# Kernel optimization log

Measured on AMD Instinct MI355X. Metric: run time of the kernel, lower is better.

The kernel has to match this reference:

```python
import jax, jax.numpy as jnp
import numpy as np

V = 32000; EMB = 128; EH = 256; DH = 256; AD = 256; BN = 512
UNK, START, END, PAD = 0, 1, 2, 3
COV_FACTOR = 1.0
B, T_IN, T_TGT = 16, 400, 100


def _lstm_cell(x, h, c, Wih, Whh, b):
    # PyTorch gate order: i, f, g, o
    g = x @ Wih.T + h @ Whh.T + b
    i, f, gg, o = jnp.split(g, 4, axis=-1)
    c = jax.nn.sigmoid(f) * c + jax.nn.sigmoid(i) * jnp.tanh(gg)
    h = jax.nn.sigmoid(o) * jnp.tanh(c)
    return h, c


def _lstm_scan(xs, Wih, Whh, b):
    # xs: [T, B, Din]
    Bz, H = xs.shape[1], Whh.shape[-1]
    def step(carry, xt):
        h, c = _lstm_cell(xt, carry[0], carry[1], Wih, Whh, b)
        return (h, c), h
    init = (jnp.zeros((Bz, H), xs.dtype), jnp.zeros((Bz, H), xs.dtype))
    (hT, cT), hs = jax.lax.scan(step, init, xs)
    return hs, hT, cT


def _bilstm(x, Wih, Whh, b):
    # x: [B, T, Din]; Wih/Whh/b stacked over direction (fwd, bwd)
    xs = jnp.swapaxes(x, 0, 1)
    hf, hTf, cTf = _lstm_scan(xs, Wih[0], Whh[0], b[0])
    hb, hTb, cTb = _lstm_scan(xs[::-1], Wih[1], Whh[1], b[1])
    out = jnp.concatenate([hf, hb[::-1]], axis=-1)  # [T, B, 2H]
    return jnp.swapaxes(out, 0, 1), jnp.concatenate([hTf, hTb], -1), jnp.concatenate([cTf, cTb], -1)


def forward_loss(emb, enc_Wih0, enc_Whh0, enc_b0, enc_Wih1, enc_Whh1, enc_b1, W_e2dh, b_e2dh, W_e2dc, b_e2dc, dec_Wih0, dec_Whh0, dec_b0, dec_Wih1, dec_Whh1, dec_b1, W_enc_attn, b_enc_attn, W_dec_attn, w_cov, v_attn, W_v1, b_v1, W_v2, b_v2, w_ctx_sw, b_ctx_sw, w_dec_sw, w_emb_sw, input_ids, target_ids, target_lengths):
    Bz, Tt = target_ids.shape
    safe_in = jnp.where(input_ids >= V, UNK, input_ids)
    x0 = emb[safe_in]                                          # [B, T_in, EMB]
    h_seq, hT0, cT0 = _bilstm(x0, enc_Wih0, enc_Whh0, enc_b0)
    enc_states, hT1, cT1 = _bilstm(h_seq, enc_Wih1, enc_Whh1, enc_b1)  # [B, T_in, 2*EH]
    hT = jnp.stack([hT0, hT1])                                 # [2, B, 2*EH] (fwd||bwd per layer)
    cT = jnp.stack([cT0, cT1])
    dec_h = hT @ W_e2dh.T + b_e2dh                             # [2, B, DH]
    dec_c = cT @ W_e2dc.T + b_e2dc
    enc_attn = enc_states @ W_enc_attn.T + b_enc_attn          # precomputed, loop-invariant
    pad_mask = input_ids == PAD
    safe_tgt = jnp.where(target_ids >= V, UNK, target_ids)
    # teacher forcing: input at t=0 is <s>, then safe(target[t-1])
    tok_in = jnp.concatenate([jnp.full((Bz, 1), START, dtype=target_ids.dtype), safe_tgt[:, :-1]], axis=1)

    def step(carry, inp):
        dh, dc, coverage, nll, cov = carry
        tok_t, tgt_t, t = inp
        e = emb[tok_t]
        h0, c0 = _lstm_cell(e, dh[0], dc[0], dec_Wih0, dec_Whh0, dec_b0)
        h1, c1 = _lstm_cell(h0, dh[1], dc[1], dec_Wih1, dec_Whh1, dec_b1)
        feat = jnp.tanh(enc_attn + (h1 @ W_dec_attn.T)[:, None, :] + coverage[..., None] * w_cov)
        scores = jnp.where(pad_mask, -jnp.inf, feat @ v_attn)
        attn = jax.nn.softmax(scores, axis=1)                  # [B, T_in]
        ctx = jnp.einsum('bt,btd->bd', attn, enc_states)
        vd = jax.nn.softmax(jax.nn.relu(jnp.concatenate([h1, ctx], axis=1) @ W_v1.T + b_v1) @ W_v2.T + b_v2, axis=1)
        # extended vocab = END left-pad zeros + generation dist (max_num_oovs = 0)
        p_vocab = jnp.take_along_axis(jnp.pad(vd, ((0, 0), (END, 0))), tgt_t[:, None], axis=1)[:, 0]
        p_gen = jax.nn.sigmoid(ctx @ w_ctx_sw + b_ctx_sw[0] + h1 @ w_dec_sw + e @ w_emb_sw)
        p_copy = jnp.sum(attn * (input_ids == tgt_t[:, None]), axis=1)
        p = p_gen * p_vocab + (1.0 - p_gen) * p_copy
        active = t < target_lengths
        nll = nll - jnp.where(active, jnp.log(p + 1e-9), 0.0)
        cov = cov + jnp.where(active, jnp.sum(jnp.minimum(attn, coverage), axis=1), 0.0)
        return (jnp.stack([h0, h1]), jnp.stack([c0, c1]), coverage + attn, nll, cov), None

    init = (dec_h, dec_c, jnp.zeros(input_ids.shape, enc_states.dtype), jnp.zeros((Bz,), enc_states.dtype), jnp.zeros((Bz,), enc_states.dtype))
    (_, _, _, nll, cov), _ = jax.lax.scan(step, init, (tok_in.T, target_ids.T, jnp.arange(Tt)))
    nll_loss = nll.sum()
    cov_loss = cov.sum()
    return jnp.stack([nll_loss, cov_loss, nll_loss + COV_FACTOR * cov_loss])


def setup_inputs() -> dict:
    ks = iter(jax.random.split(jax.random.key(0), 48))
    def w(shape, scale=0.05):
        return (jax.random.normal(next(ks), shape) * scale).astype(jnp.float32)
    def lstm_b(*shape):
        b = np.zeros(shape, np.float32)
        n = shape[-1]
        b[..., n // 4: n // 2] = 1.0  # forget-gate bias = 1 as in init_weights
        return jnp.asarray(b)
    inp = {}
    inp['batch_input_ids'] = jax.random.randint(next(ks), (B, T_IN), 0, V)
    inp['batch_target_ids'] = jax.random.randint(next(ks), (B, T_TGT), 0, V)
    inp['input_lengths'] = jnp.full((B,), T_IN, dtype=jnp.int32)  # full-length batch
    inp['target_lengths'] = jax.random.randint(next(ks), (B,), 1, T_TGT + 1)
    inp['emb'] = w((V, EMB), 0.1)
    inp['enc_Wih0'] = w((2, 4 * EH, EMB)); inp['enc_Whh0'] = w((2, 4 * EH, EH)); inp['enc_b0'] = lstm_b(2, 4 * EH)
    inp['enc_Wih1'] = w((2, 4 * EH, 2 * EH)); inp['enc_Whh1'] = w((2, 4 * EH, EH)); inp['enc_b1'] = lstm_b(2, 4 * EH)
    inp['W_e2dh'] = w((DH, 2 * EH)); inp['b_e2dh'] = jnp.zeros((DH,), jnp.float32)
    inp['W_e2dc'] = w((DH, 2 * EH)); inp['b_e2dc'] = jnp.zeros((DH,), jnp.float32)
    inp['dec_Wih0'] = w((4 * DH, EMB)); inp['dec_Whh0'] = w((4 * DH, DH)); inp['dec_b0'] = lstm_b(4 * DH)
    inp['dec_Wih1'] = w((4 * DH, DH)); inp['dec_Whh1'] = w((4 * DH, DH)); inp['dec_b1'] = lstm_b(4 * DH)
    inp['W_enc_attn'] = w((AD, 2 * EH)); inp['b_enc_attn'] = jnp.zeros((AD,), jnp.float32)
    inp['W_dec_attn'] = w((AD, DH))
    inp['w_cov'] = w((AD,))
    inp['v_attn'] = w((AD,))
    inp['W_v1'] = w((BN, DH + 2 * EH)); inp['b_v1'] = jnp.zeros((BN,), jnp.float32)
    inp['W_v2'] = w((V - END, BN)); inp['b_v2'] = jnp.zeros((V - END,), jnp.float32)
    inp['w_ctx_sw'] = w((2 * EH,)); inp['b_ctx_sw'] = jnp.zeros((1,), jnp.float32)
    inp['w_dec_sw'] = w((DH,)); inp['w_emb_sw'] = w((EMB,))
    return inp


def reference(batch_input_ids, batch_target_ids, input_lengths, target_lengths, emb, enc_Wih0, enc_Whh0, enc_b0, enc_Wih1, enc_Whh1, enc_b1, W_e2dh, b_e2dh, W_e2dc, b_e2dc, dec_Wih0, dec_Whh0, dec_b0, dec_Wih1, dec_Whh1, dec_b1, W_enc_attn, b_enc_attn, W_dec_attn, w_cov, v_attn, W_v1, b_v1, W_v2, b_v2, w_ctx_sw, b_ctx_sw, w_dec_sw, w_emb_sw):
    del input_lengths  # all sequences are full length -> pack/pad_packed is identity
    return forward_loss(emb, enc_Wih0, enc_Whh0, enc_b0, enc_Wih1, enc_Whh1, enc_b1, W_e2dh, b_e2dh, W_e2dc, b_e2dc, dec_Wih0, dec_Whh0, dec_b0, dec_Wih1, dec_Whh1, dec_b1, W_enc_attn, b_enc_attn, W_dec_attn, w_cov, v_attn, W_v1, b_v1, W_v2, b_v2, w_ctx_sw, b_ctx_sw, w_dec_sw, w_emb_sw, batch_input_ids, batch_target_ids, target_lengths)
```

## Files before the change

### kernel.cpp

```cpp
#include <hip/hip_runtime.h>
#include <hip/hip_bf16.h>

#define B    16
#define TIN  400
#define TT   100
#define EMBD 128
#define VV   32000
#define NV   31998
#define NVB  192
#define NB   256
#define LR   112
#define REP  8

__device__ __forceinline__ float sigf(float x) { return 1.f / (1.f + __expf(-x)); }
__device__ __forceinline__ float fast_tanh(float x) {
    float e = __expf(2.f * x);
    return 1.f - 2.f / (e + 1.f);
}
__device__ __forceinline__ float bflo(unsigned u) { return __uint_as_float(u << 16); }
__device__ __forceinline__ float bfhi(unsigned u) { return __uint_as_float(u & 0xffff0000u); }
__device__ __forceinline__ float bfu(unsigned short u) { return __uint_as_float((unsigned)u << 16); }
__device__ __forceinline__ unsigned short f2bf(float f) {
    unsigned u = __float_as_uint(f);
    return (unsigned short)((u + 0x7fffu + ((u >> 16) & 1u)) >> 16);
}
__device__ __forceinline__ float cldf(const float* p) {
    return __hip_atomic_load(p, __ATOMIC_RELAXED, __HIP_MEMORY_SCOPE_AGENT);
}
__device__ __forceinline__ unsigned cldu(const unsigned* p) {
    return __hip_atomic_load(p, __ATOMIC_RELAXED, __HIP_MEMORY_SCOPE_AGENT);
}
__device__ __forceinline__ unsigned long long cldu2(const unsigned long long* p) {
    return __hip_atomic_load(p, __ATOMIC_RELAXED, __HIP_MEMORY_SCOPE_AGENT);
}
__device__ __forceinline__ void stf(float* p, float v) {
    __hip_atomic_store(p, v, __ATOMIC_RELAXED, __HIP_MEMORY_SCOPE_AGENT);
}
__device__ __forceinline__ void stu(unsigned* p, unsigned v) {
    __hip_atomic_store(p, v, __ATOMIC_RELAXED, __HIP_MEMORY_SCOPE_AGENT);
}

template<int SLP>
__device__ __forceinline__ void wait_np(int* arr, int n, int ep, int tid) {
    for (int i = tid; i < n; i += 256) {
        while (__hip_atomic_load(&arr[i * 16], __ATOMIC_RELAXED, __HIP_MEMORY_SCOPE_AGENT) < ep)
            __builtin_amdgcn_s_sleep(SLP);
    }
    __syncthreads();
    asm volatile("" ::: "memory");
}
template<int SLP>
__device__ __forceinline__ void wait_line(int* l, int ep) {
    if (threadIdx.x == 0) {
        while (__hip_atomic_load(l, __ATOMIC_RELAXED, __HIP_MEMORY_SCOPE_AGENT) < ep)
            __builtin_amdgcn_s_sleep(SLP);
    }
    __syncthreads();
    asm volatile("" ::: "memory");
}
__device__ __forceinline__ void arrive(int* arr, int idx, int ep) {
    __syncthreads();
    if (threadIdx.x == 0)
        __hip_atomic_store(&arr[idx * 16], ep, __ATOMIC_RELEASE, __HIP_MEMORY_SCOPE_AGENT);
}

__global__ __launch_bounds__(256) void k_zero(float* __restrict__ p, int n) {
    int i = blockIdx.x * 256 + threadIdx.x;
    if (i < n) p[i] = 0.f;
}

__global__ __launch_bounds__(256) void k_cvt(const float* __restrict__ src, unsigned short* __restrict__ dst, int n) {
    int i = blockIdx.x * 256 + threadIdx.x;
    if (i < n) dst[i] = f2bf(src[i]);
}

__global__ __launch_bounds__(256) void k_gx0(const int* __restrict__ ids, const float* __restrict__ emb,
                                             const float* __restrict__ Wih, const float* __restrict__ bias,
                                             float* __restrict__ gx) {
// ... 44 lines not shown
        for (int b = 0; b < 16; b++) acc[b] = 0.f;
        const float4* wr = (const float4*)(W + (size_t)c * 512);
        for (int k4 = 0; k4 < 128; k4++) {
            float4 w = wr[k4];
            int k = k4 * 4;
#pragma unroll
            for (int b = 0; b < 16; b++)
                acc[b] += w.x * sx[b][k] + w.y * sx[b][k + 1] + w.z * sx[b][k + 2] + w.w * sx[b][k + 3];
        }
        float bv = bb[c];
#pragma unroll
        for (int b = 0; b < 16; b++) out[(size_t)b * 1024 + c] = acc[b] + bv;
    }
}

__global__ __launch_bounds__(256) void k_enc_layer(const float* __restrict__ gx, const float* __restrict__ Whh,
                                                   float* __restrict__ hbuf, float* __restrict__ hout,
                                                   float* __restrict__ hTs, float* __restrict__ cTs,
                                                   int* __restrict__ slots, int layer) {
    int blk = blockIdx.x;
    int dir = blk >> 4;
    int ublk = blk & 15;
    int tid = threadIdx.x;
    int rp = tid >> 3, q = tid & 7;
    int lr0 = rp * 2, lr1 = lr0 + 1;
    int g0 = lr0 & 3, g1 = lr1 & 3;
    int unit0 = ublk * 16 + (lr0 >> 2);
    int unit1 = ublk * 16 + (lr1 >> 2);
    const float* Wd = Whh + (size_t)dir * 1024 * 256;
    float wreg[64];
// ... 64 lines not shown
            float af = ((lri + 1 < 32) ? sums[(lri + 1) * 17 + bb] : sums2[((lri + 1) & 31) * 17 + bb]) + gp[1 * 256 + unit];
            float ag = ((lri + 2 < 32) ? sums[(lri + 2) * 17 + bb] : sums2[((lri + 2) & 31) * 17 + bb]) + gp[2 * 256 + unit];
            float ao = ((lri + 3 < 32) ? sums[(lri + 3) * 17 + bb] : sums2[((lri + 3) & 31) * 17 + bb]) + gp[3 * 256 + unit];
            float c = sigf(af) * creg + sigf(ai) * fast_tanh(ag);
            float h = sigf(ao) * fast_tanh(c);
            creg = c;
            stf(&hbuf[((size_t)(par ^ 1) * 2 + dir) * B * 256 + (size_t)bb * 256 + unit], h);
            if (layer == 0) hout[((size_t)t * B + bb) * 512 + dir * 256 + unit] = h;
            else            hout[((size_t)bb * TIN + t) * 512 + dir * 256 + unit] = h;
            if (s == TIN - 1) {
                hTs[((size_t)layer * B + bb) * 512 + dir * 256 + unit] = h;
                cTs[((size_t)layer * B + bb) * 512 + dir * 256 + unit] = c;
            }
        }
        int* sl = dirslots + (size_t)s * 16 * 16;
        arrive(sl, ublk, 1);
        wait_np<2>(sl, 16, 1, tid);
    }
}

__global__ __launch_bounds__(256) void k_encattn(const float* __restrict__ encs, const float* __restrict__ Wea,
                                                 const float* __restrict__ bea, unsigned short* __restrict__ encat) {
    int blk = blockIdx.x;
    __shared__ float sx[8][520];
    int tid = threadIdx.x;
    for (int i = tid; i < 8 * 512; i += 256) {
        int r = i >> 9, k = i & 511;
        sx[r][k] = encs[((size_t)blk * 8 + r) * 512 + k];
    }
    __syncthreads();
    float a[8];
    float bv = bea[tid];
// ... 34 lines not shown
    else        { h1s[(size_t)b * 256 + d] = ah; c1[(size_t)b * 256 + d] = ac; }
}

__global__ __launch_bounds__(256, 1) void k_dec_persist(
    const int* __restrict__ ids, const int* __restrict__ tgt, const int* __restrict__ tlen,
    const float* __restrict__ emb,
    const float* __restrict__ dWih0, const float* __restrict__ dWhh0, const float* __restrict__ db0,
    const float* __restrict__ dWih1, const float* __restrict__ dWhh1, const float* __restrict__ db1,
    const float* __restrict__ Wda, const float* __restrict__ wcov, const float* __restrict__ vat,
    const float* __restrict__ Wv1, const float* __restrict__ bv1,
    const unsigned short* __restrict__ W2b, const float* __restrict__ bv2,
    const float* __restrict__ wctx, const float* __restrict__ bctx,
    const float* __restrict__ wdec, const float* __restrict__ wemb,
    const unsigned short* __restrict__ ENCATH, const unsigned short* __restrict__ ENCSH,
    float* __restrict__ COVL,
    unsigned* __restrict__ CTXB, unsigned* __restrict__ FC1B,
    float* __restrict__ PCOPYR, float* __restrict__ VPARTR, float* __restrict__ LTGTR,
    float* __restrict__ H0R, const float* __restrict__ C0i,
    float* __restrict__ H1R, const float* __restrict__ C1i,
    int* __restrict__ SL, float* __restrict__ out)
{
    __shared__ float smem[39040];
    int blk = blockIdx.x, tid = threadIdx.x;
    int* B1 = SL;
    int* B2 = SL + 32 * 16;
    int* B3 = SL + 64 * 16;
    int* B4 = SL + 80 * 16;
    int* SVOC = SL + 96 * 16;
    int* SFRDY = SL + 288 * 16;
    int* FINRDY = SL + 296 * 16;

    if (blk < 32) {
        float creg0 = 0.f, creg1 = 0.f;
        if (tid < 128) {
            creg0 = C0i[(size_t)(tid & 15) * 256 + blk * 8 + (tid >> 4)];
            creg1 = C1i[(size_t)(tid & 15) * 256 + blk * 8 + (tid >> 4)];
        }
        for (int t = 0; t < TT; t++) {
            int ep = t + 1, p8 = t & 7, pm = (t + 7) & 7;
            wait_line<8>(FINRDY, t - 7);
            wait_np<2>(B2, 32, t, tid);

            for (int i = tid; i < 2048; i += 256) {
                int b = i >> 7, k = i & 127;
                int tok = (t == 0) ? 1 : tgt[b * TT + t - 1];
                if ((unsigned)tok >= VV) tok = 0;
                smem[b * 132 + k] = emb[(size_t)tok * 128 + k];
            }
            {
                const unsigned long long* s0 = (const unsigned long long*)(H0R + (size_t)pm * 4096);
                const unsigned long long* s1 = (const unsigned long long*)(H1R + (size_t)pm * 4096);
                unsigned long long v0[8], v1[8];
#pragma unroll
                for (int j = 0; j < 8; j++) v0[j] = cldu2(s0 + tid + 256 * j);
#pragma unroll
                for (int j = 0; j < 8; j++) v1[j] = cldu2(s1 + tid + 256 * j);
#pragma unroll
                for (int j = 0; j < 8; j++) {
                    int k2 = (tid + 256 * j) * 2;
                    int b = k2 >> 8, k = k2 & 255;
                    int off = b * 288 + (k >> 5) * 36 + (k & 31);
                    smem[2112 + off] = __uint_as_float((unsigned)v0[j]);
                    smem[2113 + off] = __uint_as_float((unsigned)(v0[j] >> 32));
                    smem[6720 + off] = __uint_as_float((unsigned)v1[j]);
                    smem[6721 + off] = __uint_as_float((unsigned)(v1[j] >> 32));
                }
            }
            __syncthreads();
            {
                int r = tid >> 3, q = tid & 7;
                int g = r & 3, u = r >> 2;
                int grow = g * 256 + blk * 8 + u;
                float4 wA[4], wB[8];
                const float4* wi4 = (const float4*)(dWih0 + (size_t)grow * 128 + q * 16);
                const float4* wh4 = (const float4*)(dWhh0 + (size_t)grow * 256 + q * 32);
#pragma unroll
                for (int j = 0; j < 4; j++) wA[j] = wi4[j];
#pragma unroll
                for (int j = 0; j < 8; j++) wB[j] = wh4[j];
                float pa[16];
                for (int b = 0; b < 16; b++) {
// ... 13 lines not shown
                if (q == 0)
#pragma unroll
                    for (int b = 0; b < 16; b++) smem[11328 + r * 17 + b] = pa[b];
            }
            __syncthreads();
            if (tid < 128) {
                int u = tid >> 4, b = tid & 15;
                int unit = blk * 8 + u;
                float ai = smem[11328 + (u * 4 + 0) * 17 + b] + db0[unit];
                float af = smem[11328 + (u * 4 + 1) * 17 + b] + db0[256 + unit];
                float ag = smem[11328 + (u * 4 + 2) * 17 + b] + db0[512 + unit];
                float ao = smem[11328 + (u * 4 + 3) * 17 + b] + db0[768 + unit];
                float c = sigf(af) * creg0 + sigf(ai) * fast_tanh(ag);
                float h = sigf(ao) * fast_tanh(c);
                creg0 = c;
                stf(&H0R[(size_t)p8 * 4096 + b * 256 + unit], h);
            }
            arrive(B1, blk, ep);
            wait_np<2>(B1, 32, ep, tid);
            {
                const unsigned long long* s0 = (const unsigned long long*)(H0R + (size_t)p8 * 4096);
                unsigned long long v0[8];
#pragma unroll
                for (int j = 0; j < 8; j++) v0[j] = cldu2(s0 + tid + 256 * j);
#pragma unroll
                for (int j = 0; j < 8; j++) {
                    int k2 = (tid + 256 * j) * 2;
                    int b = k2 >> 8, k = k2 & 255;
                    int off = b * 288 + (k >> 5) * 36 + (k & 31);
                    smem[2112 + off] = __uint_as_float((unsigned)v0[j]);
                    smem[2113 + off] = __uint_as_float((unsigned)(v0[j] >> 32));
                }
            }
            __syncthreads();
            {
                int r = tid >> 3, q = tid & 7;
                int g = r & 3, u = r >> 2;
                int grow = g * 256 + blk * 8 + u;
                float4 wA[8], wB[8];
                const float4* wi4 = (const float4*)(dWih1 + (size_t)grow * 256 + q * 32);
                const float4* wh4 = (const float4*)(dWhh1 + (size_t)grow * 256 + q * 32);
#pragma unroll
                for (int j = 0; j < 8; j++) { wA[j] = wi4[j]; wB[j] = wh4[j]; }
                float pa[16];
                for (int b = 0; b < 16; b++) {
                    const float4* xa = (const float4*)&smem[2112 + b * 288 + q * 36];
                    const float4* xb = (const float4*)&smem[6720 + b * 288 + q * 36];
// ... 11 lines not shown
                if (q == 0)
#pragma unroll
                    for (int b = 0; b < 16; b++) smem[11328 + r * 17 + b] = pa[b];
            }
            __syncthreads();
            if (tid < 128) {
                int u = tid >> 4, b = tid & 15;
                int unit = blk * 8 + u;
                float ai = smem[11328 + (u * 4 + 0) * 17 + b] + db1[unit];
                float af = smem[11328 + (u * 4 + 1) * 17 + b] + db1[256 + unit];
                float ag = smem[11328 + (u * 4 + 2) * 17 + b] + db1[512 + unit];
                float ao = smem[11328 + (u * 4 + 3) * 17 + b] + db1[768 + unit];
                float c = sigf(af) * creg1 + sigf(ai) * fast_tanh(ag);
                float h = sigf(ao) * fast_tanh(c);
                creg1 = c;
                stf(&H1R[(size_t)p8 * 4096 + b * 256 + unit], h);
            }
            arrive(B2, blk, ep);
        }
    } else if (blk < 48) {
        int b = blk - 32;
        float* sh1 = smem; float* sda = smem + 256; float* ssc = smem + 512;
        float* red = smem + 912; float* sred = smem + 1280; float* scov = smem + 3328;
        for (int i = tid; i < TIN; i += 256) scov[i] = 0.f;
        float covl = 0.f;
        __syncthreads();
        for (int t = 0; t < TT; t++) {
            int ep = t + 1, p8 = t & 7;
            wait_np<2>(B2, 32, ep, tid);
            if (tid < 128) {
                unsigned long long v = cldu2((const unsigned long long*)(H1R + (size_t)p8 * 4096 + b * 256) + tid);
                sh1[2 * tid] = __uint_as_float((unsigned)v);
                sh1[2 * tid + 1] = __uint_as_float((unsigned)(v >> 32));
            }
            __syncthreads();
            {
                float a = 0.f;
                const float4* wr = (const float4*)(Wda + (size_t)tid * 256);
                const float4* h4 = (const float4*)sh1;
                for (int k4 = 0; k4 < 64; k4++) {
                    float4 ww = wr[k4], x = h4[k4];
                    a += ww.x * x.x + ww.y * x.y + ww.z * x.z + ww.w * x.w;
                }
                sda[tid] = a;
            }
            __syncthreads();
            int lane = tid & 63, wv = tid >> 6;
            for (int tt = wv; tt < TIN; tt += 4) {
                float cvv = scov[tt];
                const unsigned short* ea = ENCATH + ((size_t)b * TIN + tt) * 256;
                float s4 = 0.f;
#pragma unroll
                for (int j = 0; j < 4; j++) {
                    int c = lane + 64 * j;
                    float x = bfu(ea[c]) + sda[c] + cvv * wcov[c];
                    s4 += vat[c] * fast_tanh(x);
                }
#pragma unroll
                for (int o = 32; o > 0; o >>= 1) s4 += __shfl_xor(s4, o, 64);
                if (lane == 0) ssc[tt] = (ids[b * TIN + tt] == 3) ? -1e30f : s4;
            }
            __syncthreads();
            float m = -1e30f;
            for (int i = tid; i < TIN; i += 256) m = fmaxf(m, ssc[i]);
            red[tid] = m; __syncthreads();
            for (int o = 128; o > 0; o >>= 1) { if (tid < o) red[tid] = fmaxf(red[tid], red[tid + o]); __syncthreads(); }
            m = red[0]; __syncthreads();
            float ps = 0.f;
            for (int i = tid; i < TIN; i += 256) { float ex = __expf(ssc[i] - m); ssc[i] = ex; ps += ex; }
            red[tid] = ps; __syncthreads();
            for (int o = 128; o > 0; o >>= 1) { if (tid < o) red[tid] += red[tid + o]; __syncthreads(); }
            float inv = 1.f / red[0];
            __syncthreads();
            int tgb = tgt[b * TT + t];
            float pc = 0.f, ca = 0.f;
            for (int i = tid; i < TIN; i += 256) {
                float at = ssc[i] * inv; ssc[i] = at;
                float cv = scov[i];
                ca += fminf(at, cv);
                scov[i] = cv + at;
                if (ids[b * TIN + i] == tgb) pc += at;
            }
            red[tid] = pc; __syncthreads();
            for (int o = 128; o > 0; o >>= 1) { if (tid < o) red[tid] += red[tid + o]; __syncthreads(); }
            if (tid == 0) stf(&PCOPYR[p8 * 16 + b], red[0]);
            __syncthreads();
            red[tid] = ca; __syncthreads();
            for (int o = 128; o > 0; o >>= 1) { if (tid < o) red[tid] += red[tid + o]; __syncthreads(); }
            if (tid == 0 && t < tlen[b]) covl += red[0];
            __syncthreads();
            {
                float acc[8];
#pragma unroll
                for (int j = 0; j < 8; j++) acc[j] = 0.f;
                for (int i = wv; i < TIN; i += 4) {
                    float a = ssc[i];
                    const unsigned short* es = ENCSH + ((size_t)b * TIN + i) * 512;
#pragma unroll
                    for (int j = 0; j < 8; j++) acc[j] += a * bfu(es[lane + 64 * j]);
                }
#pragma unroll
                for (int j = 0; j < 8; j++) sred[wv * 512 + 64 * j + lane] = acc[j];
                __syncthreads();
                {
                    int d2 = tid;
                    float c0 = sred[2 * d2] + sred[512 + 2 * d2] + sred[1024 + 2 * d2] + sred[1536 + 2 * d2];
                    float c1 = sred[2 * d2 + 1] + sred[512 + 2 * d2 + 1] + sred[1024 + 2 * d2 + 1] + sred[1536 + 2 * d2 + 1];
                    unsigned u = (unsigned)f2bf(c0) | ((unsigned)f2bf(c1) << 16);
                    stu(&CTXB[(size_t)p8 * 4096 + b * 256 + d2], u);
                }
            }
            if (t == TT - 1 && tid == 0) stf(&COVL[b], covl);
            arrive(B3, b, ep);
        }
    } else if (blk < 64) {
        int cb = blk - 48;
        float* Wv1s = smem;
        float* x = smem + 24576;
        float* fcout = smem + 36928;
        for (int r = 0; r < 32; r++)
            for (int k = tid; k < 768; k += 256)
                Wv1s[r * 768 + k] = Wv1[(size_t)(cb * 32 + r) * 768 + k];
        __syncthreads();
        for (int t = 0; t < TT; t++) {
            int ep = t + 1, p8 = t & 7;
            wait_np<2>(B3, 16, ep, tid);
            {
                const unsigned long long* s0 = (const unsigned long long*)(H1R + (size_t)p8 * 4096);
                unsigned long long v0[8];
#pragma unroll
                for (int j = 0; j < 8; j++) v0[j] = cldu2(s0 + tid + 256 * j);
#pragma unroll
                for (int j = 0; j < 8; j++) {
                    int k2 = (tid + 256 * j) * 2;
                    int b = k2 >> 8, k = k2 & 255;
                    x[b * 772 + k] = __uint_as_float((unsigned)v0[j]);
                    x[b * 772 + k + 1] = __uint_as_float((unsigned)(v0[j] >> 32));
                }
                const unsigned long long* s1 = (const unsigned long long*)(CTXB + (size_t)p8 * 4096);
                unsigned long long w1[8];
#pragma unroll
                for (int j = 0; j < 8; j++) w1[j] = cldu2(s1 + tid + 256 * j);
#pragma unroll
                for (int j = 0; j < 8; j++) {
                    int g = (tid + 256 * j) * 2;
                    int b = g >> 8, pj = g & 255;
                    unsigned lo = (unsigned)w1[j], hi = (unsigned)(w1[j] >> 32);
                    float* d = &x[b * 772 + 256 + 2 * pj];
                    d[0] = bflo(lo); d[1] = bfhi(lo); d[2] = bflo(hi); d[3] = bfhi(hi);
                }
            }
            __syncthreads();
            {
                int b = tid & 15, cl = tid >> 4;
                const float4* xr = (const float4*)&x[b * 772];
#pragma unroll
                for (int half = 0; half < 2; half++) {
                    int lc = half * 16 + cl;
                    float a = bv1[cb * 32 + lc];
                    const float4* wr = (const float4*)&Wv1s[lc * 768];
                    for (int k4 = 0; k4 < 192; k4++) {
                        float4 ww = wr[k4], xx = xr[k4];
                        a += ww.x * xx.x + ww.y * xx.y + ww.z * xx.z + ww.w * xx.w;
                    }
                    fcout[b * 32 + lc] = fmaxf(a, 0.f);
                }
            }
            __syncthreads();
            {
                int bb = tid >> 4, j = tid & 15;
                unsigned u = (unsigned)f2bf(fcout[bb * 32 + 2 * j]) | ((unsigned)f2bf(fcout[bb * 32 + 2 * j + 1]) << 16);
#pragma unroll
                for (int rp = 0; rp < REP; rp++)
                    stu(&FC1B[((size_t)rp * 8 + p8) * 4096 + bb * 256 + cb * 16 + j], u);
            }
            arrive(B4, cb, ep);
            if (blk == 63) {
                wait_np<2>(B4, 16, ep, tid);
                if (tid == 0) {
#pragma unroll
                    for (int rp = 0; rp < REP; rp++)
                        __hip_atomic_store(&SFRDY[rp * 16], ep, __ATOMIC_RELEASE, __HIP_MEMORY_SCOPE_AGENT);
                }
                __syncthreads();
            }
        }
    } else {
        int vb = blk - 64;
        int start = (int)(((long long)vb * NV) / NVB);
        int end   = (int)(((long long)(vb + 1) * NV) / NVB);
        float* FC1f = smem + 28672;
        float* scratch = smem + 36864;
        uint4* Wl = (uint4*)smem;
        const unsigned* myFC1B = FC1B + (size_t)(vb & 7) * 8 * 4096;
        int* mySF = &SFRDY[(vb & 7) * 16];
        float nllreg = 0.f;
        for (int i = tid; i < LR * 64; i += 256) {
            int row = i >> 6, k8 = i & 63;
            Wl[k8 * LR + row] = *(const uint4*)(W2b + (size_t)(start + row) * 512 + k8 * 8);
        }
        __syncthreads();

        for (int t = 0; t < TT; t++) {
            int ep = t + 1, p8 = t & 7;
            wait_line<4>(mySF, ep);
            {
                const unsigned long long* src = (const unsigned long long*)(myFC1B + (size_t)p8 * 4096);
                unsigned long long v[8];
#pragma unroll
                for (int j = 0; j < 8; j++) v[j] = cldu2(src + tid + 256 * j);
#pragma unroll
                for (int j = 0; j < 8; j++) {
                    int iu = tid + 256 * j;
                    unsigned lo = (unsigned)v[j], hi = (unsigned)(v[j] >> 32);
                    *(float4*)&FC1f[iu * 4] = make_float4(bflo(lo), bfhi(lo), bflo(hi), bfhi(hi));
                }
            }
            __syncthreads();
            int vl = tid & 127, kh = tid >> 7;
            float esum[16];
#pragma unroll
            for (int b = 0; b < 16; b++) esum[b] = 0.f;
            for (int chunk = 0; chunk < 2; chunk++) {
                int v = (chunk == 0) ? (start + vl) : (start + LR + vl);
                bool row_ok = (chunk == 0) ? (vl < LR) : (v < end);
                float acc[16];
#pragma unroll
                for (int b = 0; b < 16; b++) acc[b] = 0.f;
                if (row_ok) {
                    for (int k8l = 0; k8l < 32; k8l++) {
// ... 11 lines not shown
                            acc[b] += w0 * s[0] + w1 * s[1] + w2 * s[2] + w3 * s[3]
                                    + w4 * s[4] + w5 * s[5] + w6 * s[6] + w7 * s[7];
                        }
                    }
                }
                if (kh == 1 && row_ok) {
#pragma unroll
                    for (int b = 0; b < 16; b++) scratch[vl * 17 + b] = acc[b];
                }
                __syncthreads();
                if (kh == 0 && row_ok) {
                    float bias = bv2[v];
#pragma unroll
                    for (int b = 0; b < 16; b++) {
                        float lg = acc[b] + scratch[vl * 17 + b] + bias;
                        if (tgt[b * TT + t] - 2 == v) stf(&LTGTR[p8 * 16 + b], lg);
                        esum[b] += __expf(lg);
                    }
                }
                __syncthreads();
            }
            if (kh == 0) {
#pragma unroll
                for (int b = 0; b < 16; b++) scratch[vl * 17 + b] = esum[b];
            }
            __syncthreads();
            {
                int b = tid >> 4, sl = tid & 15;
                float s = 0.f;
#pragma unroll
                for (int j = 0; j < 8; j++) s += scratch[(sl + 16 * j) * 17 + b];
                FC1f[b * 17 + sl] = s;
            }
            __syncthreads();
            if (tid < 16) {
                float den = 0.f;
#pragma unroll
                for (int j = 0; j < 16; j++) den += FC1f[tid * 17 + j];
                stf(&VPARTR[(size_t)p8 * 3072 + tid * 192 + vb], den);
            }
            __syncthreads();
            arrive(SVOC, vb, ep);

            if (blk == NB - 1) {
                wait_np<2>(SVOC, NVB, ep, tid);
                float* fsc = FC1f;
                int lane = tid & 63, wv = tid >> 6;
                for (int bi = 0; bi < 4; bi++) {
                    int b = wv * 4 + bi;
                    float a = 0.f;
                    for (int k = lane; k < 256; k += 64) {
                        unsigned u = cldu(&CTXB[(size_t)p8 * 4096 + b * 256 + k]);
                        a += bflo(u) * wctx[2 * k] + bfhi(u) * wctx[2 * k + 1];
                    }
                    for (int k = lane; k < 256; k += 64) a += cldf(&H1R[(size_t)p8 * 4096 + b * 256 + k]) * wdec[k];
                    int tok = (t == 0) ? 1 : tgt[b * TT + t - 1];
                    if ((unsigned)tok >= VV) tok = 0;
                    const float* em = emb + (size_t)tok * EMBD;
                    for (int k = lane; k < 128; k += 64) a += em[k] * wemb[k];
#pragma unroll
                    for (int o = 32; o > 0; o >>= 1) a += __shfl_xor(a, o, 64);
                    if (lane == 0) fsc[300 + b] = a;
                }
                {
                    int b = tid >> 4, sl = tid & 15;
                    float s = 0.f;
                    for (int j = sl; j < NVB; j += 16) s += cldf(&VPARTR[(size_t)p8 * 3072 + b * 192 + j]);
                    fsc[b * 17 + sl] = s;
                }
                __syncthreads();
                if (tid < 16) {
                    int b = tid;
                    float den = 0.f;
#pragma unroll
                    for (int j = 0; j < 16; j++) den += fsc[b * 17 + j];
                    float pg = 1.f / (1.f + __expf(-(fsc[300 + b] + bctx[0])));
                    int tg = tgt[b * TT + t];
                    float pv = (tg >= 2) ? (__expf(cldf(&LTGTR[p8 * 16 + b])) / den) : 0.f;
                    float pr = pg * pv + (1.f - pg) * cldf(&PCOPYR[p8 * 16 + b]);
                    if (t < tlen[b]) nllreg += -logf(pr + 1e-9f);
                }
                if (t == TT - 1) {
                    if (tid < 16) fsc[340 + tid] = nllreg;
                    __syncthreads();
                    if (tid == 0) {
                        float sn = 0.f, sc = 0.f;
                        for (int b = 0; b < 16; b++) { sn += fsc[340 + b]; sc += cldf(&COVL[b]); }
                        out[0] = sn; out[1] = sc; out[2] = sn + sc;
                    }
                }
                __syncthreads();
                if (tid == 0)
                    __hip_atomic_store(FINRDY, ep, __ATOMIC_RELEASE, __HIP_MEMORY_SCOPE_AGENT);
            }
        }
    }
}

extern "C" void kernel_launch(void* const* d_in, const int* in_sizes, int n_in,
                              void* d_out, int out_size, void* d_ws, size_t ws_size,
                              hipStream_t stream) {
    (void)in_sizes; (void)n_in; (void)out_size; (void)ws_size;
    const int*   ids   = (const int*)d_in[0];
    const int*   tgt   = (const int*)d_in[1];
    const int*   tlen  = (const int*)d_in[3];
    const float* emb   = (const float*)d_in[4];
    const float* eWih0 = (const float*)d_in[5];
    const float* eWhh0 = (const float*)d_in[6];
// ... 22 lines not shown
    const float* bv2   = (const float*)d_in[29];
    const float* wctx  = (const float*)d_in[30];
    const float* bctx  = (const float*)d_in[31];
    const float* wdec  = (const float*)d_in[32];
    const float* wemb  = (const float*)d_in[33];
    float* out = (float*)d_out;

    float* ws = (float*)d_ws;
    float* GX    = ws; ws += (size_t)2 * TIN * B * 1024;
    float* HSEQ  = ws; ws += (size_t)TIN * B * 512;
    float* ENCS  = ws; ws += (size_t)B * TIN * 512;
    float* ENCATHf = ws; ws += (size_t)B * TIN * 128;
    float* ENCSHf  = ws; ws += (size_t)B * TIN * 256;
    float* HTS   = ws; ws += 2 * B * 512;
    float* CTS   = ws; ws += 2 * B * 512;
    float* H0R   = ws; ws += 8 * B * 256;
    float* C0    = ws; ws += B * 256;
    float* H1R   = ws; ws += 8 * B * 256;
    float* C1    = ws; ws += B * 256;
    float* CTXBf = ws; ws += 8 * 4096;
    float* FC1Bf = ws; ws += (size_t)REP * 8 * 4096;
    float* PCOPYR= ws; ws += 8 * B;
    float* VPARTR= ws; ws += (size_t)8 * B * NVB;
    float* LTGTR = ws; ws += 8 * B;
    float* COVL  = ws; ws += B;
    float* ZBASE = ws;
    float* EHBUF = ws; ws += 2 * 2 * B * 256;
    float* ENCSL0f = ws; ws += (size_t)2 * TIN * 16 * 16;
    float* ENCSL1f = ws; ws += (size_t)2 * TIN * 16 * 16;
    float* SLf     = ws; ws += 304 * 16;
    int zcount = (int)(ws - ZBASE);

    int* ENCSL0 = (int*)ENCSL0f;
    int* ENCSL1 = (int*)ENCSL1f;
    int* SLp    = (int*)SLf;
    unsigned short* WV2B = (unsigned short*)GX;
    unsigned short* ENCATH = (unsigned short*)ENCATHf;
    unsigned short* ENCSH  = (unsigned short*)ENCSHf;
    unsigned* CTXB = (unsigned*)CTXBf;
    unsigned* FC1B = (unsigned*)FC1Bf;

    k_zero<<<(zcount + 255) / 256, 256, 0, stream>>>(ZBASE, zcount);
    k_gx0<<<2 * TIN, 256, 0, stream>>>(ids, emb, eWih0, eb0, GX);
    k_enc_layer<<<32, 256, 0, stream>>>(GX, eWhh0, EHBUF, HSEQ, HTS, CTS, ENCSL0, 0);
    k_gx1<<<2 * TIN, 256, 0, stream>>>(HSEQ, eWih1, eb1, GX);
    k_zero<<<64, 256, 0, stream>>>(EHBUF, 2 * 2 * B * 256);
    k_enc_layer<<<32, 256, 0, stream>>>(GX, eWhh1, EHBUF, ENCS, HTS, CTS, ENCSL1, 1);
    k_cvt<<<(NV * 512 + 255) / 256, 256, 0, stream>>>(Wv2, WV2B, NV * 512);
    k_cvt<<<(B * TIN * 512 + 255) / 256, 256, 0, stream>>>(ENCS, ENCSH, B * TIN * 512);
    k_encattn<<<B * TIN / 8, 256, 0, stream>>>(ENCS, Wea, bea, ENCATH);
    k_dec_init<<<32, 256, 0, stream>>>(HTS, CTS, We2dh, be2dh, We2dc, be2dc,
                                       H0R + (size_t)7 * B * 256, C0,
                                       H1R + (size_t)7 * B * 256, C1);
    k_dec_persist<<<NB, 256, 0, stream>>>(ids, tgt, tlen, emb,
                                          dWih0, dWhh0, db0, dWih1, dWhh1, db1,
                                          Wda, wcov, vat, Wv1, bv1, WV2B, bv2,
                                          wctx, bctx, wdec, wemb,
                                          ENCATH, ENCSH, COVL, CTXB, FC1B,
                                          PCOPYR, VPARTR, LTGTR, H0R, C0, H1R, C1, SLp, out);
}
```

Measured before the change: 16.19 ms.

## Use per-timestep buffers and one-shot flags in decoder pipeline instead of ring epochs

The persistent decoder stops using 8-deep ring buffers with epoch counters and instead gives every timestep its own history buffers (hidden states, context, FC1, vocab partials) and its own set of zero-initialised flags. This drops the back-pressure wait on the final reduction block (FINRDY), so the producer stages can run ahead by any number of steps. It also removes the bf16 packing of context and the replicated FC1 copies, and stores hidden states in a transposed layout. In exchange it zeroes a much larger flag region on every call, reads more data as fp32 through plain (non-atomic) loads whose visibility depends on the release/acquire flags, and reuses part of the GX workspace for these buffers.

```diff
diff --git a/kernel.cpp b/kernel.cpp
--- a/kernel.cpp
+++ b/kernel.cpp
@@ -10,7 +10,8 @@
 #define NVB  192
 #define NB   256
 #define LR   112
-#define REP  8
+
+typedef unsigned uint4v __attribute__((ext_vector_type(4)));
 
 __device__ __forceinline__ float sigf(float x) { return 1.f / (1.f + __expf(-x)); }
 __device__ __forceinline__ float fast_tanh(float x) {
@@ -19,49 +20,45 @@
 }
 __device__ __forceinline__ float bflo(unsigned u) { return __uint_as_float(u << 16); }
 __device__ __forceinline__ float bfhi(unsigned u) { return __uint_as_float(u & 0xffff0000u); }
-__device__ __forceinline__ float bfu(unsigned short u) { return __uint_as_float((unsigned)u << 16); }
 __device__ __forceinline__ unsigned short f2bf(float f) {
     unsigned u = __float_as_uint(f);
     return (unsigned short)((u + 0x7fffu + ((u >> 16) & 1u)) >> 16);
 }
+__device__ __forceinline__ unsigned packbf(float a, float b) {
+    return (unsigned)f2bf(a) | ((unsigned)f2bf(b) << 16);
+}
 __device__ __forceinline__ float cldf(const float* p) {
     return __hip_atomic_load(p, __ATOMIC_RELAXED, __HIP_MEMORY_SCOPE_AGENT);
 }
-__device__ __forceinline__ unsigned cldu(const unsigned* p) {
-    return __hip_atomic_load(p, __ATOMIC_RELAXED, __HIP_MEMORY_SCOPE_AGENT);
-}
 __device__ __forceinline__ unsigned long long cldu2(const unsigned long long* p) {
     return __hip_atomic_load(p, __ATOMIC_RELAXED, __HIP_MEMORY_SCOPE_AGENT);
 }
 __device__ __forceinline__ void stf(float* p, float v) {
     __hip_atomic_store(p, v, __ATOMIC_RELAXED, __HIP_MEMORY_SCOPE_AGENT);
 }
-__device__ __forceinline__ void stu(unsigned* p, unsigned v) {
-    __hip_atomic_store(p, v, __ATOMIC_RELAXED, __HIP_MEMORY_SCOPE_AGENT);
-}
 
 template<int SLP>
-__device__ __forceinline__ void wait_np(int* arr, int n, int ep, int tid) {
+__device__ __forceinline__ void wait_np(int* arr, int n, int val, int tid) {
     for (int i = tid; i < n; i += 256) {
-        while (__hip_atomic_load(&arr[i * 16], __ATOMIC_RELAXED, __HIP_MEMORY_SCOPE_AGENT) < ep)
+        while (__hip_atomic_load(&arr[i * 16], __ATOMIC_RELAXED, __HIP_MEMORY_SCOPE_AGENT) < val)
             __builtin_amdgcn_s_sleep(SLP);
     }
     __syncthreads();
     asm volatile("" ::: "memory");
 }
 template<int SLP>
-__device__ __forceinline__ void wait_line(int* l, int ep) {
+__device__ __forceinline__ void wait_line(int* l, int val) {
     if (threadIdx.x == 0) {
-        while (__hip_atomic_load(l, __ATOMIC_RELAXED, __HIP_MEMORY_SCOPE_AGENT) < ep)
+        while (__hip_atomic_load(l, __ATOMIC_RELAXED, __HIP_MEMORY_SCOPE_AGENT) < val)
             __builtin_amdgcn_s_sleep(SLP);
     }
     __syncthreads();
     asm volatile("" ::: "memory");
 }
-__device__ __forceinline__ void arrive(int* arr, int idx, int ep) {
+__device__ __forceinline__ void arrive(int* arr, int idx, int val) {
     __syncthreads();
     if (threadIdx.x == 0)
-        __hip_atomic_store(&arr[idx * 16], ep, __ATOMIC_RELEASE, __HIP_MEMORY_SCOPE_AGENT);
+        __hip_atomic_store(&arr[idx * 16], val, __ATOMIC_RELEASE, __HIP_MEMORY_SCOPE_AGENT);
 }
 
 __global__ __launch_bounds__(256) void k_zero(float* __restrict__ p, int n) {
@@ -136,6 +133,19 @@
     }
 }
 
+__device__ __forceinline__ void slot_signal_e(int* sl, int idx) {
+    __syncthreads();
+    if (threadIdx.x == 0)
+        __hip_atomic_store(&sl[idx * 16], 1, __ATOMIC_RELEASE, __HIP_MEMORY_SCOPE_AGENT);
+}
+__device__ __forceinline__ void slot_wait_e(int* sl, int n, int tid) {
+    for (int i = tid; i < n; i += 256) {
+        while (__hip_atomic_load(&sl[i * 16], __ATOMIC_RELAXED, __HIP_MEMORY_SCOPE_AGENT) == 0)
+            __builtin_amdgcn_s_sleep(2);
+    }
+    __syncthreads();
+    asm volatile("" ::: "memory");
+}
 __global__ __launch_bounds__(256) void k_enc_layer(const float* __restrict__ gx, const float* __restrict__ Whh,
                                                    float* __restrict__ hbuf, float* __restrict__ hout,
                                                    float* __restrict__ hTs, float* __restrict__ cTs,
@@ -230,8 +240,8 @@
             }
         }
         int* sl = dirslots + (size_t)s * 16 * 16;
-        arrive(sl, ublk, 1);
-        wait_np<2>(sl, 16, 1, tid);
+        slot_signal_e(sl, ublk);
+        slot_wait_e(sl, 16, tid);
     }
 }
 
@@ -296,21 +306,21 @@
     const float* __restrict__ wdec, const float* __restrict__ wemb,
     const unsigned short* __restrict__ ENCATH, const unsigned short* __restrict__ ENCSH,
     float* __restrict__ COVL,
-    unsigned* __restrict__ CTXB, unsigned* __restrict__ FC1B,
-    float* __restrict__ PCOPYR, float* __restrict__ VPARTR, float* __restrict__ LTGTR,
-    float* __restrict__ H0R, const float* __restrict__ C0i,
-    float* __restrict__ H1R, const float* __restrict__ C1i,
-    int* __restrict__ SL, float* __restrict__ out)
+    float* __restrict__ H0T, float* __restrict__ H1T, float* __restrict__ CTXT,
+    unsigned* __restrict__ FC1T, float* __restrict__ VPT,
+    float* __restrict__ PCOPY, float* __restrict__ LTGT,
+    const float* __restrict__ H0I, const float* __restrict__ C0i,
+    const float* __restrict__ H1I, const float* __restrict__ C1i,
+    int* __restrict__ FLG, float* __restrict__ out)
 {
     __shared__ float smem[39040];
     int blk = blockIdx.x, tid = threadIdx.x;
-    int* B1 = SL;
-    int* B2 = SL + 32 * 16;
-    int* B3 = SL + 64 * 16;
-    int* B4 = SL + 80 * 16;
-    int* SVOC = SL + 96 * 16;
-    int* SFRDY = SL + 288 * 16;
-    int* FINRDY = SL + 296 * 16;
+    int* B1T = FLG;
+    int* B2T = FLG + 51200;
+    int* B3T = FLG + 102400;
+    int* B4T = FLG + 128000;
+    int* SFR = FLG + 153600;
+    int* SVO = FLG + 166400;
 
     if (blk < 32) {
         float creg0 = 0.f, creg1 = 0.f;
@@ -319,34 +329,26 @@
             creg1 = C1i[(size_t)(tid & 15) * 256 + blk * 8 + (tid >> 4)];
         }
         for (int t = 0; t < TT; t++) {
-            int ep = t + 1, p8 = t & 7, pm = (t + 7) & 7;
-            wait_line<8>(FINRDY, t - 7);
-            wait_np<2>(B2, 32, t, tid);
-
+            if (t > 0) wait_np<2>(B2T + (t - 1) * 512, 32, 1, tid);
             for (int i = tid; i < 2048; i += 256) {
                 int b = i >> 7, k = i & 127;
                 int tok = (t == 0) ? 1 : tgt[b * TT + t - 1];
                 if ((unsigned)tok >= VV) tok = 0;
                 smem[b * 132 + k] = emb[(size_t)tok * 128 + k];
             }
-            {
-                const unsigned long long* s0 = (const unsigned long long*)(H0R + (size_t)pm * 4096);
-                const unsigned long long* s1 = (const unsigned long long*)(H1R + (size_t)pm * 4096);
-                unsigned long long v0[8], v1[8];
-#pragma unroll
-                for (int j = 0; j < 8; j++) v0[j] = cldu2(s0 + tid + 256 * j);
-#pragma unroll
-                for (int j = 0; j < 8; j++) v1[j] = cldu2(s1 + tid + 256 * j);
-#pragma unroll
-                for (int j = 0; j < 8; j++) {
-                    int k2 = (tid + 256 * j) * 2;
-                    int b = k2 >> 8, k = k2 & 255;
-                    int off = b * 288 + (k >> 5) * 36 + (k & 31);
-                    smem[2112 + off] = __uint_as_float((unsigned)v0[j]);
-                    smem[2113 + off] = __uint_as_float((unsigned)(v0[j] >> 32));
-                    smem[6720 + off] = __uint_as_float((unsigned)v1[j]);
-                    smem[6721 + off] = __uint_as_float((unsigned)(v1[j] >> 32));
-                }
+#pragma unroll
+            for (int j = 0; j < 16; j++) {
+                int i = tid + 256 * j;
+                int b = i >> 8, k = i & 255;
+                float v0, v1;
+                if (t == 0) { v0 = H0I[b * 256 + k]; v1 = H1I[b * 256 + k]; }
+                else {
+                    v0 = H0T[(size_t)(t - 1) * 4096 + (k >> 3) * 128 + b * 8 + (k & 7)];
+                    v1 = H1T[(size_t)(t - 1) * 4096 + (k >> 3) * 128 + b * 8 + (k & 7)];
+                }
+                int off = b * 288 + (k >> 5) * 36 + (k & 31);
+                smem[2112 + off] = v0;
+                smem[6720 + off] = v1;
             }
             __syncthreads();
             {
@@ -390,23 +392,16 @@
                 float c = sigf(af) * creg0 + sigf(ai) * fast_tanh(ag);
                 float h = sigf(ao) * fast_tanh(c);
                 creg0 = c;
-                stf(&H0R[(size_t)p8 * 4096 + b * 256 + unit], h);
-            }
-            arrive(B1, blk, ep);
-            wait_np<2>(B1, 32, ep, tid);
-            {
-                const unsigned long long* s0 = (const unsigned long long*)(H0R + (size_t)p8 * 4096);
-                unsigned long long v0[8];
-#pragma unroll
-                for (int j = 0; j < 8; j++) v0[j] = cldu2(s0 + tid + 256 * j);
-#pragma unroll
-                for (int j = 0; j < 8; j++) {
-                    int k2 = (tid + 256 * j) * 2;
-                    int b = k2 >> 8, k = k2 & 255;
-                    int off = b * 288 + (k >> 5) * 36 + (k & 31);
-                    smem[2112 + off] = __uint_as_float((unsigned)v0[j]);
-                    smem[2113 + off] = __uint_as_float((unsigned)(v0[j] >> 32));
-                }
+                H0T[(size_t)t * 4096 + blk * 128 + b * 8 + u] = h;
+            }
+            arrive(B1T + t * 512, blk, 1);
+            wait_np<2>(B1T + t * 512, 32, 1, tid);
+#pragma unroll
+            for (int j = 0; j < 16; j++) {
+                int i = tid + 256 * j;
+                int b = i >> 8, k = i & 255;
+                float v0 = H0T[(size_t)t * 4096 + (k >> 3) * 128 + b * 8 + (k & 7)];
+                smem[2112 + b * 288 + (k >> 5) * 36 + (k & 31)] = v0;
             }
             __syncthreads();
             {
@@ -448,9 +443,9 @@
                 float c = sigf(af) * creg1 + sigf(ai) * fast_tanh(ag);
                 float h = sigf(ao) * fast_tanh(c);
                 creg1 = c;
-                stf(&H1R[(size_t)p8 * 4096 + b * 256 + unit], h);
-            }
-            arrive(B2, blk, ep);
+                H1T[(size_t)t * 4096 + blk * 128 + b * 8 + u] = h;
+            }
+            arrive(B2T + t * 512, blk, 1);
         }
     } else if (blk < 48) {
         int b = blk - 32;
@@ -460,13 +455,8 @@
         float covl = 0.f;
         __syncthreads();
         for (int t = 0; t < TT; t++) {
-            int ep = t + 1, p8 = t & 7;
-            wait_np<2>(B2, 32, ep, tid);
-            if (tid < 128) {
-                unsigned long long v = cldu2((const unsigned long long*)(H1R + (size_t)p8 * 4096 + b * 256) + tid);
-                sh1[2 * tid] = __uint_as_float((unsigned)v);
-                sh1[2 * tid + 1] = __uint_as_float((unsigned)(v >> 32));
-            }
+            wait_np<2>(B2T + t * 512, 32, 1, tid);
+            sh1[tid] = H1T[(size_t)t * 4096 + (tid >> 3) * 128 + b * 8 + (tid & 7)];
             __syncthreads();
             {
                 float a = 0.f;
@@ -487,7 +477,7 @@
 #pragma unroll
                 for (int j = 0; j < 4; j++) {
                     int c = lane + 64 * j;
-                    float x = bfu(ea[c]) + sda[c] + cvv * wcov[c];
+                    float x = __uint_as_float((unsigned)ea[c] << 16) + sda[c] + cvv * wcov[c];
                     s4 += vat[c] * fast_tanh(x);
                 }
 #pragma unroll
@@ -517,7 +507,7 @@
             }
             red[tid] = pc; __syncthreads();
             for (int o = 128; o > 0; o >>= 1) { if (tid < o) red[tid] += red[tid + o]; __syncthreads(); }
-            if (tid == 0) stf(&PCOPYR[p8 * 16 + b], red[0]);
+            if (tid == 0) stf(&PCOPY[t * 16 + b], red[0]);
             __syncthreads();
             red[tid] = ca; __syncthreads();
             for (int o = 128; o > 0; o >>= 1) { if (tid < o) red[tid] += red[tid + o]; __syncthreads(); }
@@ -531,21 +521,17 @@
                     float a = ssc[i];
                     const unsigned short* es = ENCSH + ((size_t)b * TIN + i) * 512;
 #pragma unroll
-                    for (int j = 0; j < 8; j++) acc[j] += a * bfu(es[lane + 64 * j]);
+                    for (int j = 0; j < 8; j++) acc[j] += a * __uint_as_float((unsigned)es[lane + 64 * j] << 16);
                 }
 #pragma unroll
                 for (int j = 0; j < 8; j++) sred[wv * 512 + 64 * j + lane] = acc[j];
                 __syncthreads();
-                {
-                    int d2 = tid;
-                    float c0 = sred[2 * d2] + sred[512 + 2 * d2] + sred[1024 + 2 * d2] + sred[1536 + 2 * d2];
-                    float c1 = sred[2 * d2 + 1] + sred[512 + 2 * d2 + 1] + sred[1024 + 2 * d2 + 1] + sred[1536 + 2 * d2 + 1];
-                    unsigned u = (unsigned)f2bf(c0) | ((unsigned)f2bf(c1) << 16);
-                    stu(&CTXB[(size_t)p8 * 4096 + b * 256 + d2], u);
-                }
+                for (int d = tid; d < 512; d += 256)
+                    CTXT[(size_t)t * 8192 + b * 512 + d] =
+                        sred[d] + sred[512 + d] + sred[1024 + d] + sred[1536 + d];
             }
             if (t == TT - 1 && tid == 0) stf(&COVL[b], covl);
-            arrive(B3, b, ep);
+            arrive(B3T + t * 256, b, 1);
         }
     } else if (blk < 64) {
         int cb = blk - 48;
@@ -557,32 +543,18 @@
                 Wv1s[r * 768 + k] = Wv1[(size_t)(cb * 32 + r) * 768 + k];
         __syncthreads();
         for (int t = 0; t < TT; t++) {
-            int ep = t + 1, p8 = t & 7;
-            wait_np<2>(B3, 16, ep, tid);
-            {
-                const unsigned long long* s0 = (const unsigned long long*)(H1R + (size_t)p8 * 4096);
-                unsigned long long v0[8];
-#pragma unroll
-                for (int j = 0; j < 8; j++) v0[j] = cldu2(s0 + tid + 256 * j);
-#pragma unroll
-                for (int j = 0; j < 8; j++) {
-                    int k2 = (tid + 256 * j) * 2;
-                    int b = k2 >> 8, k = k2 & 255;
-                    x[b * 772 + k] = __uint_as_float((unsigned)v0[j]);
-                    x[b * 772 + k + 1] = __uint_as_float((unsigned)(v0[j] >> 32));
-                }
-                const unsigned long long* s1 = (const unsigned long long*)(CTXB + (size_t)p8 * 4096);
-                unsigned long long w1[8];
-#pragma unroll
-                for (int j = 0; j < 8; j++) w1[j] = cldu2(s1 + tid + 256 * j);
-#pragma unroll
-                for (int j = 0; j < 8; j++) {
-                    int g = (tid + 256 * j) * 2;
-                    int b = g >> 8, pj = g & 255;
-                    unsigned lo = (unsigned)w1[j], hi = (unsigned)(w1[j] >> 32);
-                    float* d = &x[b * 772 + 256 + 2 * pj];
-                    d[0] = bflo(lo); d[1] = bfhi(lo); d[2] = bflo(hi); d[3] = bfhi(hi);
-                }
+            wait_np<2>(B3T + t * 256, 16, 1, tid);
+#pragma unroll
+            for (int j = 0; j < 16; j++) {
+                int i = tid + 256 * j;
+                int b = i >> 8, k = i & 255;
+                x[b * 772 + k] = H1T[(size_t)t * 4096 + (k >> 3) * 128 + b * 8 + (k & 7)];
+            }
+#pragma unroll
+            for (int j = 0; j < 8; j++) {
+                int i4 = tid + 256 * j;
+                int b = i4 >> 7, k = (i4 * 4) & 511;
+                *(float4*)&x[b * 772 + 256 + k] = *(const float4*)&CTXT[(size_t)t * 8192 + b * 512 + k];
             }
             __syncthreads();
             {
@@ -603,18 +575,16 @@
             __syncthreads();
             {
                 int bb = tid >> 4, j = tid & 15;
-                unsigned u = (unsigned)f2bf(fcout[bb * 32 + 2 * j]) | ((unsigned)f2bf(fcout[bb * 32 + 2 * j + 1]) << 16);
-#pragma unroll
-                for (int rp = 0; rp < REP; rp++)
-                    stu(&FC1B[((size_t)rp * 8 + p8) * 4096 + bb * 256 + cb * 16 + j], u);
-            }
-            arrive(B4, cb, ep);
+                FC1T[(size_t)t * 4096 + bb * 256 + cb * 16 + j] =
+                    packbf(fcout[bb * 32 + 2 * j], fcout[bb * 32 + 2 * j + 1]);
+            }
+            arrive(B4T + t * 256, cb, 1);
             if (blk == 63) {
-                wait_np<2>(B4, 16, ep, tid);
+                wait_np<2>(B4T + t * 256, 16, 1, tid);
                 if (tid == 0) {
 #pragma unroll
-                    for (int rp = 0; rp < REP; rp++)
-                        __hip_atomic_store(&SFRDY[rp * 16], ep, __ATOMIC_RELEASE, __HIP_MEMORY_SCOPE_AGENT);
+                    for (int rp = 0; rp < 8; rp++)
+                        __hip_atomic_store(&SFR[t * 128 + rp * 16], 1, __ATOMIC_RELEASE, __HIP_MEMORY_SCOPE_AGENT);
                 }
                 __syncthreads();
             }
@@ -626,8 +596,6 @@
         float* FC1f = smem + 28672;
         float* scratch = smem + 36864;
         uint4* Wl = (uint4*)smem;
-        const unsigned* myFC1B = FC1B + (size_t)(vb & 7) * 8 * 4096;
-        int* mySF = &SFRDY[(vb & 7) * 16];
         float nllreg = 0.f;
         for (int i = tid; i < LR * 64; i += 256) {
             int row = i >> 6, k8 = i & 63;
@@ -636,18 +604,19 @@
         __syncthreads();
 
         for (int t = 0; t < TT; t++) {
-            int ep = t + 1, p8 = t & 7;
-            wait_line<4>(mySF, ep);
+            wait_line<2>(&SFR[t * 128 + (vb & 7) * 16], 1);
             {
-                const unsigned long long* src = (const unsigned long long*)(myFC1B + (size_t)p8 * 4096);
-                unsigned long long v[8];
-#pragma unroll
-                for (int j = 0; j < 8; j++) v[j] = cldu2(src + tid + 256 * j);
-#pragma unroll
-                for (int j = 0; j < 8; j++) {
-                    int iu = tid + 256 * j;
-                    unsigned lo = (unsigned)v[j], hi = (unsigned)(v[j] >> 32);
-                    *(float4*)&FC1f[iu * 4] = make_float4(bflo(lo), bfhi(lo), bflo(hi), bfhi(hi));
+                const uint4v* src = (const uint4v*)(FC1T + (size_t)t * 4096);
+#pragma unroll
+                for (int j = 0; j < 4; j++) {
+                    uint4v q = src[tid + 256 * j];
+                    int i4 = tid + 256 * j;
+#pragma unroll
+                    for (int r = 0; r < 4; r++) {
+                        unsigned uu = q[r];
+                        FC1f[8 * i4 + 2 * r] = bflo(uu);
+                        FC1f[8 * i4 + 2 * r + 1] = bfhi(uu);
+                    }
                 }
             }
             __syncthreads();
@@ -689,7 +658,7 @@
 #pragma unroll
                     for (int b = 0; b < 16; b++) {
                         float lg = acc[b] + scratch[vl * 17 + b] + bias;
-                        if (tgt[b * TT + t] - 2 == v) stf(&LTGTR[p8 * 16 + b], lg);
+                        if (tgt[b * TT + t] - 2 == v) stf(&LTGT[t * 16 + b], lg);
                         esum[b] += __expf(lg);
                     }
                 }
@@ -712,23 +681,22 @@
                 float den = 0.f;
 #pragma unroll
                 for (int j = 0; j < 16; j++) den += FC1f[tid * 17 + j];
-                stf(&VPARTR[(size_t)p8 * 3072 + tid * 192 + vb], den);
-            }
-            __syncthreads();
-            arrive(SVOC, vb, ep);
+                VPT[(size_t)t * 3072 + vb * 16 + tid] = den;
+            }
+            __syncthreads();
+            arrive(SVO + t * 3072, vb, 1);
 
             if (blk == NB - 1) {
-                wait_np<2>(SVOC, NVB, ep, tid);
+                wait_np<2>(SVO + t * 3072, NVB, 1, tid);
                 float* fsc = FC1f;
                 int lane = tid & 63, wv = tid >> 6;
                 for (int bi = 0; bi < 4; bi++) {
                     int b = wv * 4 + bi;
                     float a = 0.f;
-                    for (int k = lane; k < 256; k += 64) {
-                        unsigned u = cldu(&CTXB[(size_t)p8 * 4096 + b * 256 + k]);
-                        a += bflo(u) * wctx[2 * k] + bfhi(u) * wctx[2 * k + 1];
-                    }
-                    for (int k = lane; k < 256; k += 64) a += cldf(&H1R[(size_t)p8 * 4096 + b * 256 + k]) * wdec[k];
+                    for (int k = lane; k < 512; k += 64)
+                        a += CTXT[(size_t)t * 8192 + b * 512 + k] * wctx[k];
+                    for (int k = lane; k < 256; k += 64)
+                        a += H1T[(size_t)t * 4096 + (k >> 3) * 128 + b * 8 + (k & 7)] * wdec[k];
                     int tok = (t == 0) ? 1 : tgt[b * TT + t - 1];
                     if ((unsigned)tok >= VV) tok = 0;
                     const float* em = emb + (size_t)tok * EMBD;
@@ -740,7 +708,7 @@
                 {
                     int b = tid >> 4, sl = tid & 15;
                     float s = 0.f;
-                    for (int j = sl; j < NVB; j += 16) s += cldf(&VPARTR[(size_t)p8 * 3072 + b * 192 + j]);
+                    for (int j = sl; j < NVB; j += 16) s += VPT[(size_t)t * 3072 + j * 16 + b];
                     fsc[b * 17 + sl] = s;
                 }
                 __syncthreads();
@@ -751,8 +719,8 @@
                     for (int j = 0; j < 16; j++) den += fsc[b * 17 + j];
                     float pg = 1.f / (1.f + __expf(-(fsc[300 + b] + bctx[0])));
                     int tg = tgt[b * TT + t];
-                    float pv = (tg >= 2) ? (__expf(cldf(&LTGTR[p8 * 16 + b])) / den) : 0.f;
-                    float pr = pg * pv + (1.f - pg) * cldf(&PCOPYR[p8 * 16 + b]);
+                    float pv = (tg >= 2) ? (__expf(cldf(&LTGT[t * 16 + b])) / den) : 0.f;
+                    float pr = pg * pv + (1.f - pg) * cldf(&PCOPY[t * 16 + b]);
                     if (t < tlen[b]) nllreg += -logf(pr + 1e-9f);
                 }
                 if (t == TT - 1) {
@@ -765,8 +733,6 @@
                     }
                 }
                 __syncthreads();
-                if (tid == 0)
-                    __hip_atomic_store(FINRDY, ep, __ATOMIC_RELEASE, __HIP_MEMORY_SCOPE_AGENT);
             }
         }
     }
@@ -819,31 +785,31 @@
     float* ENCSHf  = ws; ws += (size_t)B * TIN * 256;
     float* HTS   = ws; ws += 2 * B * 512;
     float* CTS   = ws; ws += 2 * B * 512;
-    float* H0R   = ws; ws += 8 * B * 256;
+    float* H0I   = ws; ws += B * 256;
     float* C0    = ws; ws += B * 256;
-    float* H1R   = ws; ws += 8 * B * 256;
+    float* H1I   = ws; ws += B * 256;
     float* C1    = ws; ws += B * 256;
-    float* CTXBf = ws; ws += 8 * 4096;
-    float* FC1Bf = ws; ws += (size_t)REP * 8 * 4096;
-    float* PCOPYR= ws; ws += 8 * B;
-    float* VPARTR= ws; ws += (size_t)8 * B * NVB;
-    float* LTGTR = ws; ws += 8 * B;
     float* COVL  = ws; ws += B;
     float* ZBASE = ws;
     float* EHBUF = ws; ws += 2 * 2 * B * 256;
     float* ENCSL0f = ws; ws += (size_t)2 * TIN * 16 * 16;
     float* ENCSL1f = ws; ws += (size_t)2 * TIN * 16 * 16;
-    float* SLf     = ws; ws += 304 * 16;
+    float* FLGf    = ws; ws += 473600;
     int zcount = (int)(ws - ZBASE);
 
     int* ENCSL0 = (int*)ENCSL0f;
     int* ENCSL1 = (int*)ENCSL1f;
-    int* SLp    = (int*)SLf;
+    int* FLG    = (int*)FLGf;
     unsigned short* WV2B = (unsigned short*)GX;
+    float* H0T  = GX + 8191488;
+    float* H1T  = GX + 8601088;
+    float* CTXT = GX + 9010688;
+    unsigned* FC1T = (unsigned*)(GX + 9829888);
+    float* VPT  = GX + 10239488;
+    float* PCOPY= GX + 10546688;
+    float* LTGT = GX + 10548288;
     unsigned short* ENCATH = (unsigned short*)ENCATHf;
     unsigned short* ENCSH  = (unsigned short*)ENCSHf;
-    unsigned* CTXB = (unsigned*)CTXBf;
-    unsigned* FC1B = (unsigned*)FC1Bf;
 
     k_zero<<<(zcount + 255) / 256, 256, 0, stream>>>(ZBASE, zcount);
     k_gx0<<<2 * TIN, 256, 0, stream>>>(ids, emb, eWih0, eb0, GX);
@@ -854,13 +820,12 @@
     k_cvt<<<(NV * 512 + 255) / 256, 256, 0, stream>>>(Wv2, WV2B, NV * 512);
     k_cvt<<<(B * TIN * 512 + 255) / 256, 256, 0, stream>>>(ENCS, ENCSH, B * TIN * 512);
     k_encattn<<<B * TIN / 8, 256, 0, stream>>>(ENCS, Wea, bea, ENCATH);
-    k_dec_init<<<32, 256, 0, stream>>>(HTS, CTS, We2dh, be2dh, We2dc, be2dc,
-                                       H0R + (size_t)7 * B * 256, C0,
-                                       H1R + (size_t)7 * B * 256, C1);
+    k_dec_init<<<32, 256, 0, stream>>>(HTS, CTS, We2dh, be2dh, We2dc, be2dc, H0I, C0, H1I, C1);
     k_dec_persist<<<NB, 256, 0, stream>>>(ids, tgt, tlen, emb,
                                           dWih0, dWhh0, db0, dWih1, dWhh1, db1,
                                           Wda, wcov, vat, Wv1, bv1, WV2B, bv2,
                                           wctx, bctx, wdec, wemb,
-                                          ENCATH, ENCSH, COVL, CTXB, FC1B,
-                                          PCOPYR, VPARTR, LTGTR, H0R, C0, H1R, C1, SLp, out);
-}
+                                          ENCATH, ENCSH, COVL,
+                                          H0T, H1T, CTXT, FC1T, VPT, PCOPY, LTGT,
+                                          H0I, C0, H1I, C1, FLG, out);
+}
```

Result: no change. 15.92 ms (-1.7%).
